# Optimization experiments

Measured on AMD Instinct MI355X. Metric: run time of the kernel, lower is better.

Reference implementation:

```python
import jax, jax.numpy as jnp
import numpy as np

N_NODES = 131072
BATCH = 128
H = 256


def setup_inputs() -> dict:
    key = jax.random.key(0)
    k1, k2, k3, k4 = jax.random.split(key, 4)
    node_features = jax.random.normal(k1, (N_NODES, H), dtype=jnp.float32)
    # strictly increasing offsets (root indices) so no segment is empty
    offsets = jnp.sort(jax.random.randint(k2, (BATCH,), 0, N_NODES - BATCH)) + jnp.arange(BATCH)
    offsets = offsets.astype(jnp.int64)
    W1 = jax.random.normal(k3, (H, H), dtype=jnp.float32) / np.sqrt(H)
    b1 = jnp.zeros((H,), dtype=jnp.float32)
    W2 = jax.random.normal(k4, (H, 1), dtype=jnp.float32) / np.sqrt(H)
    b2 = jnp.zeros((1,), dtype=jnp.float32)
    return {"node_features": node_features, "offsets": offsets,
            "W1": W1, "b1": b1, "W2": W2, "b2": b2}


def _segment_bounds(offsets, n_nodes):
    # Faithful to the torch loop:
    #   i == 0       : [offsets[0],   offsets[1])
    #   0 < i < B-1  : [offsets[i-1], offsets[i+1])
    #   i == B-1     : [offsets[B-2], n_nodes)
    B = offsets.shape[0]
    starts = jnp.concatenate([offsets[:1], offsets[:-1]])          # (B,)
    ends = jnp.concatenate([offsets[2:], jnp.array([n_nodes, n_nodes], dtype=offsets.dtype)])
    if B == 1:
        starts = jnp.zeros((1,), offsets.dtype)
        ends = jnp.full((1,), n_nodes, offsets.dtype)
    return starts, ends


def reference(node_features, offsets, W1, b1, W2, b2):
    N = node_features.shape[0]
    # attention MLP scores for every node, computed once: (N,)
    scores = (jnp.tanh(node_features @ W1 + b1) @ W2 + b2)[:, 0]
    starts, ends = _segment_bounds(offsets, N)
    idx = jnp.arange(N)
    mask = (idx[None, :] >= starts[:, None]) & (idx[None, :] < ends[:, None])  # (B, N)
    logits = jnp.where(mask, scores[None, :], jnp.float32(-1e30))
    attn = jax.nn.softmax(logits, axis=1)              # (B, N), zero outside segment
    return attn @ node_features                        # (B, H)
```

## Files before the change

kernel.cpp:

```cpp
#include <hip/hip_runtime.h>
#include <hip/hip_bf16.h>

#define N_NODES 131072
#define BATCH 128
#define H 256
#define NTILES (N_NODES / 64)

typedef _Float16 half8 __attribute__((ext_vector_type(8)));
typedef _Float16 half4 __attribute__((ext_vector_type(4)));
typedef float floatx4 __attribute__((ext_vector_type(4)));

__global__ __launch_bounds__(256) void prep_kernel(
    const float* __restrict__ W1, _Float16* __restrict__ W1p,
    float* __restrict__ pacc, float* __restrict__ pz)
{
    const int bid = blockIdx.x;
    const int tid = threadIdx.x;
    if (bid < 32) {
        const int g = bid * 256 + tid;
        const int ct = g >> 9;
        const int ks = (g >> 6) & 7;
        const int l  = g & 63;
        const int k0 = ks * 32 + (l >> 4) * 8;
        const int col = ct * 16 + (l & 15);
        half8 h;
        #pragma unroll
        for (int j = 0; j < 8; ++j) h[j] = (_Float16)W1[(k0 + j) * H + col];
        reinterpret_cast<half8*>(W1p)[g] = h;
    } else {
        pacc[(bid - 32) * 256 + tid] = 0.f;
        if (bid == 32 && tid < BATCH) pz[tid] = 0.f;
    }
}

__global__ __launch_bounds__(256, 4) void fused_kernel(
    const float* __restrict__ X, const _Float16* __restrict__ W1p,
    const float* __restrict__ b1, const float* __restrict__ W2,
    const float* __restrict__ b2, const int* __restrict__ offsets,
    float* __restrict__ pacc, float* __restrict__ pz)
{
    __shared__ __align__(16) _Float16 Xs[64 * H];
    __shared__ float sp[4][64];
    __shared__ float scL[64];
    __shared__ float accL[4][H];
    __shared__ float zLs[4];
    __shared__ int offL[BATCH];

    const int tid = threadIdx.x;
    const int wave = tid >> 6;
    const int lane = tid & 63;
    const int t0 = blockIdx.x * 64;

    if (tid < BATCH) offL[tid] = offsets[tid];

    {
        const float4* Xv = reinterpret_cast<const float4*>(X + (long long)t0 * H);
        #pragma unroll
        for (int i = 0; i < 8; ++i) {
            const int c = tid + i * 256;
            const int row = c >> 5;
            const int col8 = c & 31;
            float4 a  = Xv[row * 64 + col8 * 2];
            float4 bq = Xv[row * 64 + col8 * 2 + 1];
            half8 h;
            h[0] = (_Float16)a.x;  h[1] = (_Float16)a.y;
            h[2] = (_Float16)a.z;  h[3] = (_Float16)a.w;
            h[4] = (_Float16)bq.x; h[5] = (_Float16)bq.y;
            h[6] = (_Float16)bq.z; h[7] = (_Float16)bq.w;
            int byte = row * 512 + col8 * 16;
            byte ^= (row & 7) << 4;
            *reinterpret_cast<half8*>(reinterpret_cast<char*>(Xs) + byte) = h;
        }
    }
    __syncthreads();

    floatx4 acc[4][4];
    #pragma unroll
    for (int rt = 0; rt < 4; ++rt)
        #pragma unroll
        for (int ctl = 0; ctl < 4; ++ctl)
            acc[rt][ctl] = (floatx4){0.f, 0.f, 0.f, 0.f};

    const half8* Bw = reinterpret_cast<const half8*>(W1p) + wave * 2048 + lane;

    #pragma unroll 2
    for (int ks = 0; ks < 8; ++ks) {
        half8 bf0 = Bw[ks * 64];
        half8 bf1 = Bw[512 + ks * 64];
        half8 bf2 = Bw[1024 + ks * 64];
        half8 bf3 = Bw[1536 + ks * 64];
        half8 af[4];
        #pragma unroll
        for (int rt = 0; rt < 4; ++rt) {
            const int row = rt * 16 + (lane & 15);
            int byte = row * 512 + ks * 64 + (lane >> 4) * 16;
            byte ^= (row & 7) << 4;
            af[rt] = *reinterpret_cast<const half8*>(
                reinterpret_cast<const char*>(Xs) + byte);
        }
        #pragma unroll
        for (int rt = 0; rt < 4; ++rt) {
            acc[rt][0] = __builtin_amdgcn_mfma_f32_16x16x32_f16(af[rt], bf0, acc[rt][0], 0, 0, 0);
            acc[rt][1] = __builtin_amdgcn_mfma_f32_16x16x32_f16(af[rt], bf1, acc[rt][1], 0, 0, 0);
            acc[rt][2] = __builtin_amdgcn_mfma_f32_16x16x32_f16(af[rt], bf2, acc[rt][2], 0, 0, 0);
            acc[rt][3] = __builtin_amdgcn_mfma_f32_16x16x32_f16(af[rt], bf3, acc[rt][3], 0, 0, 0);
        }
    }

    float w2v[4], b1v[4];
    #pragma unroll
    for (int ctl = 0; ctl < 4; ++ctl) {
        const int col = wave * 64 + ctl * 16 + (lane & 15);
        w2v[ctl] = W2[col];
        b1v[ctl] = b1[col];
    }

    float sc[4][4];
    #pragma unroll
    for (int rt = 0; rt < 4; ++rt) {
        #pragma unroll
        for (int reg = 0; reg < 4; ++reg) {
            float s = 0.f;
            #pragma unroll
            for (int ctl = 0; ctl < 4; ++ctl) {
                const float x = acc[rt][ctl][reg] + b1v[ctl];
                const float t = 1.f - 2.f / (__expf(2.f * x) + 1.f);
                s = fmaf(t, w2v[ctl], s);
            }
            sc[rt][reg] = s;
        }
    }
    #pragma unroll
    for (int off = 1; off < 16; off <<= 1)
        #pragma unroll
        for (int rt = 0; rt < 4; ++rt)
            #pragma unroll
            for (int reg = 0; reg < 4; ++reg)
                sc[rt][reg] += __shfl_xor(sc[rt][reg], off);

    if ((lane & 15) == 0) {
        #pragma unroll
        for (int rt = 0; rt < 4; ++rt)
            #pragma unroll
            for (int reg = 0; reg < 4; ++reg)
                sp[wave][rt * 16 + (lane >> 4) * 4 + reg] = sc[rt][reg];
    }
    __syncthreads();
    if (tid < 64)
        scL[tid] = __expf(sp[0][tid] + sp[1][tid] + sp[2][tid] + sp[3][tid] + b2[0]);
    __syncthreads();

    int g_lo, g_hi;
    {
        int node = t0;
        if (node < offL[0]) g_lo = -1;
        else {
            int lo = 0, hi = BATCH - 1;
            while (lo < hi) { int mid = (lo + hi + 1) >> 1; if (offL[mid] <= node) lo = mid; else hi = mid - 1; }
            g_lo = lo;
        }
        node = t0 + 63;
        if (node < offL[0]) g_hi = -1;
        else {
            int lo = 0, hi = BATCH - 1;
            while (lo < hi) { int mid = (lo + hi + 1) >> 1; if (offL[mid] <= node) lo = mid; else hi = mid - 1; }
            g_hi = lo;
        }
    }

    for (int g = (g_lo < 0 ? 0 : g_lo); g <= g_hi; ++g) {
        const int rs = max(t0, offL[g]);
        const int re = min(t0 + 64, (g == BATCH - 1) ? N_NODES : offL[g + 1]);

        float4 a4 = {0.f, 0.f, 0.f, 0.f};
        float z = 0.f;
        for (int i = rs + wave; i < re; i += 4) {
            const int r = i - t0;
            const float p = scL[r];
            const int byte = r * 512 + ((((lane >> 1) ^ (r & 7))) << 4) + (lane & 1) * 8;
            half4 xv = *reinterpret_cast<const half4*>(
                reinterpret_cast<const char*>(Xs) + byte);
            a4.x = fmaf(p, (float)xv[0], a4.x);
            a4.y = fmaf(p, (float)xv[1], a4.y);
            a4.z = fmaf(p, (float)xv[2], a4.z);
            a4.w = fmaf(p, (float)xv[3], a4.w);
            z += p;
        }
        reinterpret_cast<float4*>(&accL[wave][0])[lane] = a4;
        if (lane == 0) zLs[wave] = z;
        __syncthreads();
        const float v = accL[0][tid] + accL[1][tid] + accL[2][tid] + accL[3][tid];
        atomicAdd(&pacc[g * H + tid], v);
        if (tid == 0) atomicAdd(&pz[g], zLs[0] + zLs[1] + zLs[2] + zLs[3]);
        __syncthreads();
    }
}

__global__ __launch_bounds__(256) void reduce_kernel(
    const float* __restrict__ pacc, const float* __restrict__ pz,
    float* __restrict__ out)
{
    const int b = blockIdx.x;
    const int tid = threadIdx.x;
    const int g0 = (b == 0) ? 0 : b - 1;
    const int g1 = (b >= BATCH - 1) ? BATCH - 1 : b + 1;

    float r = 0.f, z = 0.f;
    for (int g = g0; g <= g1; ++g) {
        r += pacc[g * H + tid];
        z += pz[g];
    }
    out[b * H + tid] = r / z;
}

extern "C" void kernel_launch(void* const* d_in, const int* in_sizes, int n_in,
                              void* d_out, int out_size, void* d_ws, size_t ws_size,
                              hipStream_t stream)
{
    const float* X     = (const float*)d_in[0];
    const int* offs    = (const int*)d_in[1];
    const float* W1    = (const float*)d_in[2];
    const float* b1    = (const float*)d_in[3];
    const float* W2    = (const float*)d_in[4];
    const float* b2    = (const float*)d_in[5];
    float* out         = (float*)d_out;

    float* pacc   = (float*)d_ws;
    float* pz     = pacc + BATCH * H;
    _Float16* W1p = (_Float16*)(pz + BATCH);

    prep_kernel<<<160, 256, 0, stream>>>(W1, W1p, pacc, pz);
    fused_kernel<<<NTILES, 256, 0, stream>>>(X, W1p, b1, W2, b2, offs, pacc, pz);
    reduce_kernel<<<BATCH, 256, 0, stream>>>(pacc, pz, out);
}
```

Measured before the change: 61.24 us.

## Make fused kernel persistent over four tiles with register prefetch of next tile

Each block now processes four consecutive 64-node tiles instead of one. While the current tile is converted to fp16 in LDS, the next tile's X rows are loaded into registers, so global loads overlap with MFMA and softmax work. Per-segment partial sums are kept across tiles and flushed with atomics only when the segment changes, which cuts the number of atomics. Block IDs are also remapped across XCDs. In exchange it uses more registers (launch bounds lowered to 2 blocks per CU) and the grid shrinks to 512 blocks, so there is less parallelism.

```diff
diff --git a/kernel.cpp b/kernel.cpp
--- a/kernel.cpp
+++ b/kernel.cpp
@@ -4,7 +4,8 @@
 #define N_NODES 131072
 #define BATCH 128
 #define H 256
-#define NTILES (N_NODES / 64)
+#define TPB 4
+#define GRID 512
 
 typedef _Float16 half8 __attribute__((ext_vector_type(8)));
 typedef _Float16 half4 __attribute__((ext_vector_type(4)));
@@ -33,7 +34,7 @@
     }
 }
 
-__global__ __launch_bounds__(256, 4) void fused_kernel(
+__global__ __launch_bounds__(256, 2) void fused_kernel(
     const float* __restrict__ X, const _Float16* __restrict__ W1p,
     const float* __restrict__ b1, const float* __restrict__ W2,
     const float* __restrict__ b2, const int* __restrict__ offsets,
@@ -49,61 +50,24 @@
     const int tid = threadIdx.x;
     const int wave = tid >> 6;
     const int lane = tid & 63;
-    const int t0 = blockIdx.x * 64;
+
+    const int bid = (int)(blockIdx.x & 7) * (GRID / 8) + (int)(blockIdx.x >> 3);
+    const int tbase = bid * TPB;
 
     if (tid < BATCH) offL[tid] = offsets[tid];
 
+    const float4* X4 = reinterpret_cast<const float4*>(X);
+
+    float4 va[8], vb[8];
     {
-        const float4* Xv = reinterpret_cast<const float4*>(X + (long long)t0 * H);
+        const float4* Xv = X4 + (long long)tbase * 64 * 64;
         #pragma unroll
         for (int i = 0; i < 8; ++i) {
             const int c = tid + i * 256;
             const int row = c >> 5;
             const int col8 = c & 31;
-            float4 a  = Xv[row * 64 + col8 * 2];
-            float4 bq = Xv[row * 64 + col8 * 2 + 1];
-            half8 h;
-            h[0] = (_Float16)a.x;  h[1] = (_Float16)a.y;
-            h[2] = (_Float16)a.z;  h[3] = (_Float16)a.w;
-            h[4] = (_Float16)bq.x; h[5] = (_Float16)bq.y;
-            h[6] = (_Float16)bq.z; h[7] = (_Float16)bq.w;
-            int byte = row * 512 + col8 * 16;
-            byte ^= (row & 7) << 4;
-            *reinterpret_cast<half8*>(reinterpret_cast<char*>(Xs) + byte) = h;
-        }
-    }
-    __syncthreads();
-
-    floatx4 acc[4][4];
-    #pragma unroll
-    for (int rt = 0; rt < 4; ++rt)
-        #pragma unroll
-        for (int ctl = 0; ctl < 4; ++ctl)
-            acc[rt][ctl] = (floatx4){0.f, 0.f, 0.f, 0.f};
-
-    const half8* Bw = reinterpret_cast<const half8*>(W1p) + wave * 2048 + lane;
-
-    #pragma unroll 2
-    for (int ks = 0; ks < 8; ++ks) {
-        half8 bf0 = Bw[ks * 64];
-        half8 bf1 = Bw[512 + ks * 64];
-        half8 bf2 = Bw[1024 + ks * 64];
-        half8 bf3 = Bw[1536 + ks * 64];
-        half8 af[4];
-        #pragma unroll
-        for (int rt = 0; rt < 4; ++rt) {
-            const int row = rt * 16 + (lane & 15);
-            int byte = row * 512 + ks * 64 + (lane >> 4) * 16;
-            byte ^= (row & 7) << 4;
-            af[rt] = *reinterpret_cast<const half8*>(
-                reinterpret_cast<const char*>(Xs) + byte);
-        }
-        #pragma unroll
-        for (int rt = 0; rt < 4; ++rt) {
-            acc[rt][0] = __builtin_amdgcn_mfma_f32_16x16x32_f16(af[rt], bf0, acc[rt][0], 0, 0, 0);
-            acc[rt][1] = __builtin_amdgcn_mfma_f32_16x16x32_f16(af[rt], bf1, acc[rt][1], 0, 0, 0);
-            acc[rt][2] = __builtin_amdgcn_mfma_f32_16x16x32_f16(af[rt], bf2, acc[rt][2], 0, 0, 0);
-            acc[rt][3] = __builtin_amdgcn_mfma_f32_16x16x32_f16(af[rt], bf3, acc[rt][3], 0, 0, 0);
+            va[i] = Xv[row * 64 + col8 * 2];
+            vb[i] = Xv[row * 64 + col8 * 2 + 1];
         }
     }
 
@@ -114,86 +78,163 @@
         w2v[ctl] = W2[col];
         b1v[ctl] = b1[col];
     }
-
-    float sc[4][4];
-    #pragma unroll
-    for (int rt = 0; rt < 4; ++rt) {
-        #pragma unroll
-        for (int reg = 0; reg < 4; ++reg) {
-            float s = 0.f;
-            #pragma unroll
-            for (int ctl = 0; ctl < 4; ++ctl) {
-                const float x = acc[rt][ctl][reg] + b1v[ctl];
-                const float t = 1.f - 2.f / (__expf(2.f * x) + 1.f);
-                s = fmaf(t, w2v[ctl], s);
-            }
-            sc[rt][reg] = s;
-        }
-    }
-    #pragma unroll
-    for (int off = 1; off < 16; off <<= 1)
+    const float bias2 = b2[0];
+
+    const half8* Bw = reinterpret_cast<const half8*>(W1p) + wave * 2048 + lane;
+
+    float4 a4 = {0.f, 0.f, 0.f, 0.f};
+    float zacc = 0.f;
+    int g_cur = -1;
+
+    auto flushFn = [&]() {
+        reinterpret_cast<float4*>(&accL[wave][0])[lane] = a4;
+        if (lane == 0) zLs[wave] = zacc;
+        __syncthreads();
+        const float v = accL[0][tid] + accL[1][tid] + accL[2][tid] + accL[3][tid];
+        atomicAdd(&pacc[g_cur * H + tid], v);
+        if (tid == 0) atomicAdd(&pz[g_cur], zLs[0] + zLs[1] + zLs[2] + zLs[3]);
+        __syncthreads();
+        a4 = (float4){0.f, 0.f, 0.f, 0.f};
+        zacc = 0.f;
+    };
+
+    for (int t = 0; t < TPB; ++t) {
+        const int t0 = (tbase + t) * 64;
+
+        #pragma unroll
+        for (int i = 0; i < 8; ++i) {
+            const int c = tid + i * 256;
+            const int row = c >> 5;
+            const int col8 = c & 31;
+            half8 h;
+            h[0] = (_Float16)va[i].x; h[1] = (_Float16)va[i].y;
+            h[2] = (_Float16)va[i].z; h[3] = (_Float16)va[i].w;
+            h[4] = (_Float16)vb[i].x; h[5] = (_Float16)vb[i].y;
+            h[6] = (_Float16)vb[i].z; h[7] = (_Float16)vb[i].w;
+            int byte = row * 512 + col8 * 16;
+            byte ^= (row & 7) << 4;
+            *reinterpret_cast<half8*>(reinterpret_cast<char*>(Xs) + byte) = h;
+        }
+        if (t < TPB - 1) {
+            const float4* Xv = X4 + (long long)(tbase + t + 1) * 64 * 64;
+            #pragma unroll
+            for (int i = 0; i < 8; ++i) {
+                const int c = tid + i * 256;
+                const int row = c >> 5;
+                const int col8 = c & 31;
+                va[i] = Xv[row * 64 + col8 * 2];
+                vb[i] = Xv[row * 64 + col8 * 2 + 1];
+            }
+        }
+        __syncthreads();
+
+        floatx4 acc[4][4];
         #pragma unroll
         for (int rt = 0; rt < 4; ++rt)
             #pragma unroll
-            for (int reg = 0; reg < 4; ++reg)
-                sc[rt][reg] += __shfl_xor(sc[rt][reg], off);
-
-    if ((lane & 15) == 0) {
-        #pragma unroll
-        for (int rt = 0; rt < 4; ++rt)
-            #pragma unroll
-            for (int reg = 0; reg < 4; ++reg)
-                sp[wave][rt * 16 + (lane >> 4) * 4 + reg] = sc[rt][reg];
-    }
-    __syncthreads();
-    if (tid < 64)
-        scL[tid] = __expf(sp[0][tid] + sp[1][tid] + sp[2][tid] + sp[3][tid] + b2[0]);
-    __syncthreads();
-
-    int g_lo, g_hi;
-    {
-        int node = t0;
-        if (node < offL[0]) g_lo = -1;
-        else {
-            int lo = 0, hi = BATCH - 1;
-            while (lo < hi) { int mid = (lo + hi + 1) >> 1; if (offL[mid] <= node) lo = mid; else hi = mid - 1; }
-            g_lo = lo;
-        }
-        node = t0 + 63;
-        if (node < offL[0]) g_hi = -1;
-        else {
-            int lo = 0, hi = BATCH - 1;
-            while (lo < hi) { int mid = (lo + hi + 1) >> 1; if (offL[mid] <= node) lo = mid; else hi = mid - 1; }
-            g_hi = lo;
-        }
-    }
-
-    for (int g = (g_lo < 0 ? 0 : g_lo); g <= g_hi; ++g) {
-        const int rs = max(t0, offL[g]);
-        const int re = min(t0 + 64, (g == BATCH - 1) ? N_NODES : offL[g + 1]);
-
-        float4 a4 = {0.f, 0.f, 0.f, 0.f};
-        float z = 0.f;
-        for (int i = rs + wave; i < re; i += 4) {
-            const int r = i - t0;
-            const float p = scL[r];
-            const int byte = r * 512 + ((((lane >> 1) ^ (r & 7))) << 4) + (lane & 1) * 8;
-            half4 xv = *reinterpret_cast<const half4*>(
-                reinterpret_cast<const char*>(Xs) + byte);
-            a4.x = fmaf(p, (float)xv[0], a4.x);
-            a4.y = fmaf(p, (float)xv[1], a4.y);
-            a4.z = fmaf(p, (float)xv[2], a4.z);
-            a4.w = fmaf(p, (float)xv[3], a4.w);
-            z += p;
-        }
-        reinterpret_cast<float4*>(&accL[wave][0])[lane] = a4;
-        if (lane == 0) zLs[wave] = z;
-        __syncthreads();
-        const float v = accL[0][tid] + accL[1][tid] + accL[2][tid] + accL[3][tid];
-        atomicAdd(&pacc[g * H + tid], v);
-        if (tid == 0) atomicAdd(&pz[g], zLs[0] + zLs[1] + zLs[2] + zLs[3]);
-        __syncthreads();
-    }
+            for (int ctl = 0; ctl < 4; ++ctl)
+                acc[rt][ctl] = (floatx4){0.f, 0.f, 0.f, 0.f};
+
+        #pragma unroll 2
+        for (int ks = 0; ks < 8; ++ks) {
+            half8 bf0 = Bw[ks * 64];
+            half8 bf1 = Bw[512 + ks * 64];
+            half8 bf2 = Bw[1024 + ks * 64];
+            half8 bf3 = Bw[1536 + ks * 64];
+            half8 af[4];
+            #pragma unroll
+            for (int rt = 0; rt < 4; ++rt) {
+                const int row = rt * 16 + (lane & 15);
+                int byte = row * 512 + ks * 64 + (lane >> 4) * 16;
+                byte ^= (row & 7) << 4;
+                af[rt] = *reinterpret_cast<const half8*>(
+                    reinterpret_cast<const char*>(Xs) + byte);
+            }
+            #pragma unroll
+            for (int rt = 0; rt < 4; ++rt) {
+                acc[rt][0] = __builtin_amdgcn_mfma_f32_16x16x32_f16(af[rt], bf0, acc[rt][0], 0, 0, 0);
+                acc[rt][1] = __builtin_amdgcn_mfma_f32_16x16x32_f16(af[rt], bf1, acc[rt][1], 0, 0, 0);
+                acc[rt][2] = __builtin_amdgcn_mfma_f32_16x16x32_f16(af[rt], bf2, acc[rt][2], 0, 0, 0);
+                acc[rt][3] = __builtin_amdgcn_mfma_f32_16x16x32_f16(af[rt], bf3, acc[rt][3], 0, 0, 0);
+            }
+        }
+
+        float sc[4][4];
+        #pragma unroll
+        for (int rt = 0; rt < 4; ++rt) {
+            #pragma unroll
+            for (int reg = 0; reg < 4; ++reg) {
+                float s = 0.f;
+                #pragma unroll
+                for (int ctl = 0; ctl < 4; ++ctl) {
+                    const float x = acc[rt][ctl][reg] + b1v[ctl];
+                    const float tt = 1.f - 2.f / (__expf(2.f * x) + 1.f);
+                    s = fmaf(tt, w2v[ctl], s);
+                }
+                sc[rt][reg] = s;
+            }
+        }
+        #pragma unroll
+        for (int off = 1; off < 16; off <<= 1)
+            #pragma unroll
+            for (int rt = 0; rt < 4; ++rt)
+                #pragma unroll
+                for (int reg = 0; reg < 4; ++reg)
+                    sc[rt][reg] += __shfl_xor(sc[rt][reg], off);
+
+        if ((lane & 15) == 0) {
+            #pragma unroll
+            for (int rt = 0; rt < 4; ++rt)
+                #pragma unroll
+                for (int reg = 0; reg < 4; ++reg)
+                    sp[wave][rt * 16 + (lane >> 4) * 4 + reg] = sc[rt][reg];
+        }
+        __syncthreads();
+        if (tid < 64)
+            scL[tid] = __expf(sp[0][tid] + sp[1][tid] + sp[2][tid] + sp[3][tid] + bias2);
+        __syncthreads();
+
+        int g_lo, g_hi;
+        {
+            int node = t0;
+            if (node < offL[0]) g_lo = -1;
+            else {
+                int lo = 0, hi = BATCH - 1;
+                while (lo < hi) { int mid = (lo + hi + 1) >> 1; if (offL[mid] <= node) lo = mid; else hi = mid - 1; }
+                g_lo = lo;
+            }
+            node = t0 + 63;
+            if (node < offL[0]) g_hi = -1;
+            else {
+                int lo = 0, hi = BATCH - 1;
+                while (lo < hi) { int mid = (lo + hi + 1) >> 1; if (offL[mid] <= node) lo = mid; else hi = mid - 1; }
+                g_hi = lo;
+            }
+        }
+
+        for (int g = (g_lo < 0 ? 0 : g_lo); g <= g_hi; ++g) {
+            if (g != g_cur) {
+                if (g_cur >= 0) flushFn();
+                g_cur = g;
+            }
+            const int rs = max(t0, offL[g]);
+            const int re = min(t0 + 64, (g == BATCH - 1) ? N_NODES : offL[g + 1]);
+            for (int i = rs + wave; i < re; i += 4) {
+                const int r = i - t0;
+                const float p = scL[r];
+                const int byte = r * 512 + ((((lane >> 1) ^ (r & 7))) << 4) + (lane & 1) * 8;
+                half4 xv = *reinterpret_cast<const half4*>(
+                    reinterpret_cast<const char*>(Xs) + byte);
+                a4.x = fmaf(p, (float)xv[0], a4.x);
+                a4.y = fmaf(p, (float)xv[1], a4.y);
+                a4.z = fmaf(p, (float)xv[2], a4.z);
+                a4.w = fmaf(p, (float)xv[3], a4.w);
+                zacc += p;
+            }
+        }
+        __syncthreads();
+    }
+    if (g_cur >= 0) flushFn();
 }
 
 __global__ __launch_bounds__(256) void reduce_kernel(
@@ -230,6 +271,6 @@
     _Float16* W1p = (_Float16*)(pz + BATCH);
 
     prep_kernel<<<160, 256, 0, stream>>>(W1, W1p, pacc, pz);
-    fused_kernel<<<NTILES, 256, 0, stream>>>(X, W1p, b1, W2, b2, offs, pacc, pz);
+    fused_kernel<<<GRID, 256, 0, stream>>>(X, W1p, b1, W2, b2, offs, pacc, pz);
     reduce_kernel<<<BATCH, 256, 0, stream>>>(pacc, pz, out);
 }
```

Result: slower. 63.03 us (+2.9%).

## Repartition MFMA work per wave by rows, drop cross-wave reductions, swizzle blocks

Applied to the files above, without the earlier changes.

Each wave now computes all 256 output columns for its own 16 rows, not 64 columns for all 64 rows. The score reduction therefore stays inside the wave, and the shared scratch and one barrier go away. The per-segment pooling now issues per-wave global atomics directly instead of reducing across waves in shared memory behind two barriers. Block indices are also remapped in strides across the grid. The cost is more global loads of W1 fragments per wave (each wave reads the full W1), four times as many atomics to the same addresses, and the loop is no longer unrolled.

```diff
diff --git a/kernel.cpp b/kernel.cpp
--- a/kernel.cpp
+++ b/kernel.cpp
@@ -40,16 +40,15 @@
     float* __restrict__ pacc, float* __restrict__ pz)
 {
     __shared__ __align__(16) _Float16 Xs[64 * H];
-    __shared__ float sp[4][64];
     __shared__ float scL[64];
-    __shared__ float accL[4][H];
-    __shared__ float zLs[4];
     __shared__ int offL[BATCH];
 
     const int tid = threadIdx.x;
     const int wave = tid >> 6;
     const int lane = tid & 63;
-    const int t0 = blockIdx.x * 64;
+
+    const int bid = (int)(blockIdx.x & 7) * (NTILES / 8) + (int)(blockIdx.x >> 3);
+    const int t0 = bid * 64;
 
     if (tid < BATCH) offL[tid] = offsets[tid];
 
@@ -67,87 +66,65 @@
             h[2] = (_Float16)a.z;  h[3] = (_Float16)a.w;
             h[4] = (_Float16)bq.x; h[5] = (_Float16)bq.y;
             h[6] = (_Float16)bq.z; h[7] = (_Float16)bq.w;
-            int byte = row * 512 + col8 * 16;
-            byte ^= (row & 7) << 4;
+            int byte = row * 512 + (col8 * 16 ^ ((row & 7) << 4));
             *reinterpret_cast<half8*>(reinterpret_cast<char*>(Xs) + byte) = h;
         }
     }
     __syncthreads();
 
-    floatx4 acc[4][4];
+    floatx4 acc[16];
     #pragma unroll
-    for (int rt = 0; rt < 4; ++rt)
-        #pragma unroll
-        for (int ctl = 0; ctl < 4; ++ctl)
-            acc[rt][ctl] = (floatx4){0.f, 0.f, 0.f, 0.f};
-
-    const half8* Bw = reinterpret_cast<const half8*>(W1p) + wave * 2048 + lane;
-
-    #pragma unroll 2
+    for (int ct = 0; ct < 16; ++ct) acc[ct] = (floatx4){0.f, 0.f, 0.f, 0.f};
+
+    const half8* Bv = reinterpret_cast<const half8*>(W1p) + lane;
+    const int arow = wave * 16 + (lane & 15);
+    const int aswz = (arow & 7) << 4;
+    const char* XsRow = reinterpret_cast<const char*>(Xs) + arow * 512;
+    const int acolbase = (lane >> 4) * 16;
+
+    #pragma unroll 1
     for (int ks = 0; ks < 8; ++ks) {
-        half8 bf0 = Bw[ks * 64];
-        half8 bf1 = Bw[512 + ks * 64];
-        half8 bf2 = Bw[1024 + ks * 64];
-        half8 bf3 = Bw[1536 + ks * 64];
-        half8 af[4];
-        #pragma unroll
-        for (int rt = 0; rt < 4; ++rt) {
-            const int row = rt * 16 + (lane & 15);
-            int byte = row * 512 + ks * 64 + (lane >> 4) * 16;
-            byte ^= (row & 7) << 4;
-            af[rt] = *reinterpret_cast<const half8*>(
-                reinterpret_cast<const char*>(Xs) + byte);
-        }
-        #pragma unroll
-        for (int rt = 0; rt < 4; ++rt) {
-            acc[rt][0] = __builtin_amdgcn_mfma_f32_16x16x32_f16(af[rt], bf0, acc[rt][0], 0, 0, 0);
-            acc[rt][1] = __builtin_amdgcn_mfma_f32_16x16x32_f16(af[rt], bf1, acc[rt][1], 0, 0, 0);
-            acc[rt][2] = __builtin_amdgcn_mfma_f32_16x16x32_f16(af[rt], bf2, acc[rt][2], 0, 0, 0);
-            acc[rt][3] = __builtin_amdgcn_mfma_f32_16x16x32_f16(af[rt], bf3, acc[rt][3], 0, 0, 0);
-        }
-    }
-
-    float w2v[4], b1v[4];
+        half8 af = *reinterpret_cast<const half8*>(
+            XsRow + ((ks * 64 + acolbase) ^ aswz));
+        half8 bf[8];
+        #pragma unroll
+        for (int ct = 0; ct < 8; ++ct) bf[ct] = Bv[(ct * 8 + ks) * 64];
+        #pragma unroll
+        for (int ct = 0; ct < 8; ++ct)
+            acc[ct] = __builtin_amdgcn_mfma_f32_16x16x32_f16(af, bf[ct], acc[ct], 0, 0, 0);
+        #pragma unroll
+        for (int ct = 0; ct < 8; ++ct) bf[ct] = Bv[((ct + 8) * 8 + ks) * 64];
+        #pragma unroll
+        for (int ct = 0; ct < 8; ++ct)
+            acc[ct + 8] = __builtin_amdgcn_mfma_f32_16x16x32_f16(af, bf[ct], acc[ct + 8], 0, 0, 0);
+    }
+
+    float s[4] = {0.f, 0.f, 0.f, 0.f};
     #pragma unroll
-    for (int ctl = 0; ctl < 4; ++ctl) {
-        const int col = wave * 64 + ctl * 16 + (lane & 15);
-        w2v[ctl] = W2[col];
-        b1v[ctl] = b1[col];
-    }
-
-    float sc[4][4];
-    #pragma unroll
-    for (int rt = 0; rt < 4; ++rt) {
+    for (int ct = 0; ct < 16; ++ct) {
+        const int col = ct * 16 + (lane & 15);
+        const float b1c = b1[col];
+        const float w2c = W2[col];
         #pragma unroll
         for (int reg = 0; reg < 4; ++reg) {
-            float s = 0.f;
-            #pragma unroll
-            for (int ctl = 0; ctl < 4; ++ctl) {
-                const float x = acc[rt][ctl][reg] + b1v[ctl];
-                const float t = 1.f - 2.f / (__expf(2.f * x) + 1.f);
-                s = fmaf(t, w2v[ctl], s);
-            }
-            sc[rt][reg] = s;
+            const float x = acc[ct][reg] + b1c;
+            const float t = 1.f - 2.f / (__expf(2.f * x) + 1.f);
+            s[reg] = fmaf(t, w2c, s[reg]);
         }
     }
     #pragma unroll
     for (int off = 1; off < 16; off <<= 1)
         #pragma unroll
-        for (int rt = 0; rt < 4; ++rt)
-            #pragma unroll
-            for (int reg = 0; reg < 4; ++reg)
-                sc[rt][reg] += __shfl_xor(sc[rt][reg], off);
+        for (int reg = 0; reg < 4; ++reg)
+            s[reg] += __shfl_xor(s[reg], off);
 
     if ((lane & 15) == 0) {
-        #pragma unroll
-        for (int rt = 0; rt < 4; ++rt)
-            #pragma unroll
-            for (int reg = 0; reg < 4; ++reg)
-                sp[wave][rt * 16 + (lane >> 4) * 4 + reg] = sc[rt][reg];
-    }
-    __syncthreads();
-    if (tid < 64)
-        scL[tid] = __expf(sp[0][tid] + sp[1][tid] + sp[2][tid] + sp[3][tid] + b2[0]);
+        const float bias2 = b2[0];
+        const int r0 = wave * 16 + (lane >> 4) * 4;
+        #pragma unroll
+        for (int reg = 0; reg < 4; ++reg)
+            scL[r0 + reg] = __expf(s[reg] + bias2);
+    }
     __syncthreads();
 
     int g_lo, g_hi;
@@ -186,13 +163,12 @@
             a4.w = fmaf(p, (float)xv[3], a4.w);
             z += p;
         }
-        reinterpret_cast<float4*>(&accL[wave][0])[lane] = a4;
-        if (lane == 0) zLs[wave] = z;
-        __syncthreads();
-        const float v = accL[0][tid] + accL[1][tid] + accL[2][tid] + accL[3][tid];
-        atomicAdd(&pacc[g * H + tid], v);
-        if (tid == 0) atomicAdd(&pz[g], zLs[0] + zLs[1] + zLs[2] + zLs[3]);
-        __syncthreads();
+        float* dst = &pacc[g * H + lane * 4];
+        atomicAdd(dst + 0, a4.x);
+        atomicAdd(dst + 1, a4.y);
+        atomicAdd(dst + 2, a4.z);
+        atomicAdd(dst + 3, a4.w);
+        if (lane == 0) atomicAdd(&pz[g], z);
     }
 }
 
```

Measured after the change: 164.5 us. +168.6%, slower.
